# Kernel tuning notes

Measured on AMD Instinct MI355X. Metric: run time of the kernel, lower is better.

The kernel has to match this reference:

```python
import jax, jax.numpy as jnp
import numpy as np

B, L, D, H, DFF, C = 16, 1024, 256, 4, 2048, 3
NS, NC = 4, 4
DH = D // H


def _ln(x, g, b):
    m = x.mean(-1, keepdims=True)
    v = ((x - m) ** 2).mean(-1, keepdims=True)
    return (x - m) / jnp.sqrt(v + 1e-5) * g + b


def setup_inputs() -> dict:
    key = jax.random.key(0)
    ks = jax.random.split(key, 24)
    n = lambda k, s: jax.random.normal(k, s, jnp.float32) * 0.02
    return {
        'shape_idxs': jax.random.randint(ks[0], (B, L), 0, NS, jnp.int32),
        'color_idxs': jax.random.randint(ks[1], (B, L), 0, NC, jnp.int32),
        'shape_emb': n(ks[2], (NS, D)),
        'color_emb': n(ks[3], (NC, D)),
        'Wq': n(ks[4], (D, D)), 'bq': jnp.zeros((D,)),
        'Wk': n(ks[5], (D, D)), 'bk': jnp.zeros((D,)),
        'Wv': n(ks[6], (D, D)), 'bv': jnp.zeros((D,)),
        'Wo': n(ks[7], (D, D)), 'bo': jnp.zeros((D,)),
        'g1': jnp.ones((D,)), 'be1': jnp.zeros((D,)),
        'W1': n(ks[8], (D, DFF)), 'bf1': jnp.zeros((DFF,)),
        'W2': n(ks[9], (DFF, D)), 'bf2': jnp.zeros((D,)),
        'g2': jnp.ones((D,)), 'be2': jnp.zeros((D,)),
        'Wl': n(ks[10], (D, C)), 'bl': jnp.zeros((C,)),
        'Wp1': n(ks[11], (D, D)), 'bp1': jnp.zeros((D,)),
        'Wp2': n(ks[12], (D, 1)), 'bp2': jnp.zeros((1,)),
        'wc': n(ks[13], (1, 1)), 'bc': jnp.zeros((1,)),
    }


def reference(shape_idxs, color_idxs, shape_emb, color_emb, Wq, bq, Wk, bk, Wv, bv,
              Wo, bo, g1, be1, W1, bf1, W2, bf2, g2, be2, Wl, bl,
              Wp1, bp1, Wp2, bp2, wc, bc):
    # embed (dropout is identity in eval)
    x = shape_emb[shape_idxs] + color_emb[color_idxs]  # [B,L,D]
    # post-norm transformer encoder layer (PyTorch default)
    heads = lambda t: t.reshape(B, L, H, DH)
    q, k, v = heads(x @ Wq + bq), heads(x @ Wk + bk), heads(x @ Wv + bv)
    scores = jnp.einsum('blhd,bmhd->bhlm', q, k) / jnp.sqrt(jnp.float32(DH))
    attn = jax.nn.softmax(scores, axis=-1)
    ctx = jnp.einsum('bhlm,bmhd->blhd', attn, v).reshape(B, L, D)
    y = _ln(x + ctx @ Wo + bo, g1, be1)
    ff = jax.nn.relu(y @ W1 + bf1) @ W2 + bf2
    y = _ln(y + ff, g2, be2)  # trans_out [B,L,D]
    # latent logits / KL(prior || probs) with batchmean reduction
    logits = y @ Wl + bl
    logp = jax.nn.log_softmax(logits, axis=-1)
    prior = 1.0 / C
    kl_loss = jnp.sum(prior * (jnp.log(jnp.float32(prior)) - logp)) / B
    # data-dependent boundary segmentation (argmax of probs == argmax of logits)
    boundaries = (jnp.argmax(logits, axis=-1) == 0)
    boundaries = boundaries.at[:, 0].set(True)
    closed = boundaries & (jnp.arange(L) > 0)  # closure at l>0 ends segment at l
    seg_id = jnp.cumsum(closed.astype(jnp.int32), axis=1) - closed  # exclusive cumsum
    gid = (jnp.arange(B)[:, None] * L + seg_id).reshape(-1)  # global segment ids
    sums = jax.ops.segment_sum(y.reshape(B * L, D), gid, num_segments=B * L)
    counts = jax.ops.segment_sum(jnp.ones((B * L,), jnp.float32), gid, num_segments=B * L)
    means = sums / jnp.maximum(counts, 1.0)[:, None]  # per-segment mean [B*L,D]
    # predicate net + composition, mean over valid segments
    preds = jax.nn.sigmoid(jax.nn.relu(means @ Wp1 + bp1) @ Wp2 + bp2)  # [B*L,1]
    comp = (preds * wc[0, 0] + bc[0]).reshape(B, L)
    valid = (counts > 0).reshape(B, L).astype(jnp.float32)
    mean_comp = jnp.sum(comp * valid, axis=1) / jnp.sum(valid, axis=1)
    final_scores = jax.nn.sigmoid(mean_comp)
    return final_scores, kl_loss
```

## Files before the change

### kernel.cpp

```cpp
#include <hip/hip_runtime.h>


typedef unsigned short u16;
typedef u16    u16x4  __attribute__((ext_vector_type(4)));
typedef u16    u16x8  __attribute__((ext_vector_type(8)));
typedef __bf16 bf16x8 __attribute__((ext_vector_type(8)));
typedef float  f32x4  __attribute__((ext_vector_type(4)));

__device__ __forceinline__ float bf2f(u16 u) {
    union { unsigned int i; float f; } v; v.i = ((unsigned int)u) << 16; return v.f;
}
__device__ __forceinline__ u16 f2bf(float f) {
    union { float f; unsigned int i; } v; v.f = f;
    unsigned int r = (v.i + 0x7FFFu + ((v.i >> 16) & 1u)) >> 16;
    return (u16)r;
}
__device__ __forceinline__ u16 f2bf_fast(float f) {
    union { __bf16 h; u16 u; } v; v.h = (__bf16)f; return v.u;
}
__device__ __forceinline__ void gll16(const u16* g, u16* l) {
    __builtin_amdgcn_global_load_lds((__attribute__((address_space(1))) void*)(u16*)g,
                                     (__attribute__((address_space(3))) void*)l, 16, 0, 0);
}

__global__ void k_dzero(int* __restrict__ diag) {
    if (threadIdx.x < 16) diag[threadIdx.x] = 0;
}
__global__ __launch_bounds__(256) void k_detect(const u16* __restrict__ w1raw,
                                                int* __restrict__ diag) {
    int i = blockIdx.x * 256 + threadIdx.x;
    int bad = 0;
    for (int k = i; k < 65536; k += 64 * 256) {
        unsigned v = w1raw[k] & 0x7FFFu;
        if (v >= 0x7F80u) bad++;
    }
    for (int off = 32; off >= 1; off >>= 1) bad += __shfl_xor(bad, off);
    __shared__ int bs[4];
    if ((threadIdx.x & 63) == 0) bs[threadIdx.x >> 6] = bad;
    __syncthreads();
    if (threadIdx.x == 0) {
        int tot = bs[0] + bs[1] + bs[2] + bs[3];
        if (tot) atomicAdd(&diag[14], tot);
        __threadfence();
        int ticket = atomicAdd(&diag[13], 1);
        if (ticket == 63) {
            int cnt = atomicAdd(&diag[14], 0);
            diag[15] = (cnt > 16) ? 1 : 0;
        }
    }
}

struct IngestTab {
    const void* src[26];
    unsigned    dstoff[26];
    int         n[26];
    float       scale[26];
};
__global__ __launch_bounds__(256) void k_ingest(IngestTab tab, u16* __restrict__ ing,
                                                const int* __restrict__ diag) {
    int t = blockIdx.y;
    int n = tab.n[t];
    int m = diag[15];
    float sc = tab.scale[t];
    u16* dst = ing + tab.dstoff[t];
    for (int i = blockIdx.x * 256 + threadIdx.x; i < n; i += gridDim.x * 256) {
        float v = m ? ((const float*)tab.src[t])[i] : bf2f(((const u16*)tab.src[t])[i]);
        dst[i] = f2bf(v * sc);
    }
}
__global__ void k_sentinel_f32(float* __restrict__ out, int code) {
    int t = threadIdx.x;
    if (t < 17) out[t] = (float)code;
}

struct TransTab {
    const u16* src[7];
    u16*       dst[7];
    int        K[7], N[7];
    int        tstart[8];
};
__global__ __launch_bounds__(256) void k_trans_all(TransTab tt) {
    __shared__ u16 tile[32][33];
    int bx = blockIdx.x;
    int wgt = 0;
#pragma unroll
    for (int i = 1; i < 7; ++i) if (bx >= tt.tstart[i]) wgt = i;
    int local = bx - tt.tstart[wgt];
    int K = tt.K[wgt], N = tt.N[wgt];
    int ntx = N >> 5;
    int txt = local % ntx, tyt = local / ntx;
    const u16* W = tt.src[wgt];
    u16* Wt = tt.dst[wgt];
    int tx = threadIdx.x & 31, ty = threadIdx.x >> 5;
    int n = txt * 32 + tx;
    for (int i = ty; i < 32; i += 8) {
        int k = tyt * 32 + i;
        tile[i][tx] = W[(size_t)k * N + n];
    }
    __syncthreads();
    int k2 = tyt * 32 + tx;
    for (int i = ty; i < 32; i += 8) {
        int n2 = txt * 32 + i;
        Wt[(size_t)n2 * K + k2] = tile[tx][i];
    }
}

__global__ __launch_bounds__(256) void k_vt(const u16* __restrict__ QKV,
                                            u16* __restrict__ VT) {
    __shared__ u16 tile[32][33];
    int tx = threadIdx.x & 31, ty = threadIdx.x >> 5;
    int bh = blockIdx.y >> 1, dh = blockIdx.y & 1;
    int b = bh >> 2, h = bh & 3;
    int l0 = blockIdx.x * 32, d0 = dh * 32;
    const u16* src = QKV + (size_t)(b * 1024 + l0) * 768 + 512 + h * 64 + d0;
    for (int i = ty; i < 32; i += 8)
        tile[i][tx] = src[(size_t)i * 768 + tx];
    __syncthreads();
    u16* dst = VT + (size_t)(bh * 64 + d0) * 1024 + l0;
    for (int i = ty; i < 32; i += 8)
        dst[(size_t)i * 1024 + tx] = tile[tx][i];
}

__global__ __launch_bounds__(256) void k_embed(const int* __restrict__ si,
                                               const int* __restrict__ ci,
                                               const u16* __restrict__ se,
                                               const u16* __restrict__ ce,
                                               u16* __restrict__ X) {
    int t = blockIdx.x * 256 + threadIdx.x;
    int row = t >> 5, seg = (t & 31) * 8;
    int s = si[row], c = ci[row];
    u16x8 a = *(const u16x8*)&se[s * 256 + seg];
    u16x8 b = *(const u16x8*)&ce[c * 256 + seg];
    u16x8 o;
#pragma unroll
    for (int e = 0; e < 8; ++e) o[e] = f2bf(bf2f(a[e]) + bf2f(b[e]));
    *(u16x8*)&X[(size_t)row * 256 + seg] = o;
}

__global__ __launch_bounds__(256) void k_gemm_bt(const u16* __restrict__ A,
                                                 const u16* __restrict__ Bt,
                                                 const u16* __restrict__ bias,
                                                 u16* __restrict__ C,
                                                 int N, int K, int relu, int gx) {
    __shared__ u16 As[128][32];
    __shared__ u16 Bs[128][32];
    const int tid = threadIdx.x;
    const int xcd = blockIdx.x & 7, j = blockIdx.x >> 3;
    const int m0 = (xcd * 16 + j / gx) * 128, n0 = (j % gx) * 128;
    const int lane = tid & 63, wid = tid >> 6;
    const int wm = (wid & 1) * 64, wn = (wid >> 1) * 64;
    const int m16 = lane & 15, quad = lane >> 4;
    f32x4 acc[4][4] = {};
    const int arow = tid >> 2;
    const int ac8  = (tid & 3) * 8;
    const u16* Ap0 = A  + (size_t)(m0 + arow) * K + ac8;
    const u16* Ap1 = A  + (size_t)(m0 + 64 + arow) * K + ac8;
    const u16* Bp0 = Bt + (size_t)(n0 + arow) * K + ac8;
    const u16* Bp1 = Bt + (size_t)(n0 + 64 + arow) * K + ac8;
    u16* lA0 = &As[arow][ac8];
    u16* lA1 = &As[64 + arow][ac8];
    u16* lB0 = &Bs[arow][ac8];
    u16* lB1 = &Bs[64 + arow][ac8];

    for (int k0 = 0; k0 < K; k0 += 32) {
        __syncthreads();
        gll16(Ap0 + k0, lA0);
        gll16(Ap1 + k0, lA1);
        gll16(Bp0 + k0, lB0);
        gll16(Bp1 + k0, lB1);
        __syncthreads();
        bf16x8 af[4], bfv[4];
#pragma unroll
        for (int i = 0; i < 4; ++i)
            af[i] = *(const bf16x8*)&As[wm + i * 16 + m16][quad * 8];
#pragma unroll
        for (int j2 = 0; j2 < 4; ++j2)
            bfv[j2] = *(const bf16x8*)&Bs[wn + j2 * 16 + m16][quad * 8];
#pragma unroll
        for (int i = 0; i < 4; ++i)
#pragma unroll
            for (int j2 = 0; j2 < 4; ++j2)
                acc[i][j2] = __builtin_amdgcn_mfma_f32_16x16x32_bf16(
                    af[i], bfv[j2], acc[i][j2], 0, 0, 0);
    }

#pragma unroll
    for (int i = 0; i < 4; ++i) {
        int row = m0 + wm + i * 16 + quad * 4;
#pragma unroll
        for (int j2 = 0; j2 < 4; ++j2) {
            int col = n0 + wn + j2 * 16 + m16;
            float bv = bf2f(bias[col]);
#pragma unroll
            for (int r = 0; r < 4; ++r) {
                float v = acc[i][j2][r] + bv;
                if (relu) v = fmaxf(v, 0.f);
                C[(size_t)(row + r) * N + col] = f2bf_fast(v);
            }
        }
    }
}

__global__ __launch_bounds__(256) void k_gemm64(const u16* __restrict__ A,
                                                const u16* __restrict__ Bt,
                                                const u16* __restrict__ bias,
                                                u16* __restrict__ C,
                                                int N, int K, int relu,
                                                int gx, int mtpx,
                                                const float* __restrict__ gate) {
    __shared__ u16 As0[64][32], As1[64][32];
    __shared__ u16 Bs0[128][32], Bs1[128][32];
    const int tid = threadIdx.x;
    const int xcd = blockIdx.x & 7, j = blockIdx.x >> 3;
    const int m0 = (xcd * mtpx + j / gx) * 64, n0 = (j % gx) * 128;
    if (gate && gate[m0] == 0.f) return;
    const int lane = tid & 63, wid = tid >> 6;
    const int wm = (wid & 1) * 32, wn = (wid >> 1) * 64;
    const int m16 = lane & 15, quad = lane >> 4;
    f32x4 acc[2][4] = {};
    const int arow = tid >> 2;
    const int ac8  = (tid & 3) * 8;
    const u16* Ap  = A  + (size_t)(m0 + arow) * K + ac8;
    const u16* Bp0 = Bt + (size_t)(n0 + arow) * K + ac8;
    const u16* Bp1 = Bt + (size_t)(n0 + 64 + arow) * K + ac8;
    u16* lA0  = &As0[arow][ac8];
    u16* lA1  = &As1[arow][ac8];
    u16* lB00 = &Bs0[arow][ac8];
    u16* lB01 = &Bs0[64 + arow][ac8];
    u16* lB10 = &Bs1[arow][ac8];
    u16* lB11 = &Bs1[64 + arow][ac8];

    for (int k0 = 0; k0 < K; k0 += 64) {
        __syncthreads();
        gll16(Ap + k0,        lA0);
        gll16(Ap + k0 + 32,   lA1);
        gll16(Bp0 + k0,       lB00);
        gll16(Bp0 + k0 + 32,  lB10);
        gll16(Bp1 + k0,       lB01);
        gll16(Bp1 + k0 + 32,  lB11);
        __syncthreads();
#pragma unroll
        for (int ks = 0; ks < 2; ++ks) {
            bf16x8 af[2], bfv[4];
#pragma unroll
            for (int i = 0; i < 2; ++i)
                af[i] = ks == 0 ? *(const bf16x8*)&As0[wm + i * 16 + m16][quad * 8]
                                : *(const bf16x8*)&As1[wm + i * 16 + m16][quad * 8];
#pragma unroll
            for (int j2 = 0; j2 < 4; ++j2)
                bfv[j2] = ks == 0 ? *(const bf16x8*)&Bs0[wn + j2 * 16 + m16][quad * 8]
                                  : *(const bf16x8*)&Bs1[wn + j2 * 16 + m16][quad * 8];
#pragma unroll
            for (int i = 0; i < 2; ++i)
#pragma unroll
                for (int j2 = 0; j2 < 4; ++j2)
                    acc[i][j2] = __builtin_amdgcn_mfma_f32_16x16x32_bf16(
                        af[i], bfv[j2], acc[i][j2], 0, 0, 0);
        }
    }

#pragma unroll
    for (int i = 0; i < 2; ++i) {
        int row = m0 + wm + i * 16 + quad * 4;
#pragma unroll
        for (int j2 = 0; j2 < 4; ++j2) {
            int col = n0 + wn + j2 * 16 + m16;
            float bv = bf2f(bias[col]);
#pragma unroll
            for (int r = 0; r < 4; ++r) {
                float v = acc[i][j2][r] + bv;
                if (relu) v = fmaxf(v, 0.f);
                C[(size_t)(row + r) * N + col] = f2bf_fast(v);
            }
        }
    }
}

__global__ __launch_bounds__(256) void k_attn_mfma(const u16* __restrict__ QKV,
                                                   const u16* __restrict__ VT,
                                                   u16* __restrict__ CTX) {
    __shared__ u16 Ks[64][72];
    __shared__ u16 Vts[64][72];
    __shared__ u16 Ps[4][16][72];
    const int tid = threadIdx.x, lane = tid & 63, w = tid >> 6;
    const int quad = lane >> 4, c = lane & 15;
    const int blk = blockIdx.x;
    const int xcd = blk & 7, local = blk >> 3;
    const int bh = xcd * 8 + (local >> 4);
    const int qt = local & 15;
    const int b = bh >> 2, h = bh & 3;
    const int qrow0 = b * 1024 + qt * 64;

    const u16* qptr = QKV + (size_t)(qrow0 + w * 16 + c) * 768 + h * 64;
    bf16x8 aq0 = *(const bf16x8*)(qptr + quad * 8);
    bf16x8 aq1 = *(const bf16x8*)(qptr + 32 + quad * 8);

    f32x4 acc_o[4] = {};
    float l_part[4] = {0.f, 0.f, 0.f, 0.f};

    const u16* kbase  = QKV + (size_t)(b * 1024) * 768 + 256 + h * 64;
    const u16* vtbase = VT + (size_t)(bh * 64) * 1024;
    const int skk = tid >> 3, sc8 = (tid & 7) * 8;

    for (int t = 0; t < 16; ++t) {
        __syncthreads();
#pragma unroll
        for (int it = 0; it < 2; ++it) {
            int rr = skk + 32 * it;
            *(u16x8*)&Ks[rr][sc8]  = *(const u16x8*)(kbase + (size_t)(t * 64 + rr) * 768 + sc8);
            *(u16x8*)&Vts[rr][sc8] = *(const u16x8*)(vtbase + (size_t)rr * 1024 + t * 64 + sc8);
        }
        __syncthreads();

        f32x4 s[4];
#pragma unroll
        for (int nt = 0; nt < 4; ++nt) {
            f32x4 z = {};
            bf16x8 bk0 = *(const bf16x8*)&Ks[nt * 16 + c][quad * 8];
            bf16x8 bk1 = *(const bf16x8*)&Ks[nt * 16 + c][32 + quad * 8];
            z = __builtin_amdgcn_mfma_f32_16x16x32_bf16(aq0, bk0, z, 0, 0, 0);
            s[nt] = __builtin_amdgcn_mfma_f32_16x16x32_bf16(aq1, bk1, z, 0, 0, 0);
        }

#pragma unroll
        for (int nt = 0; nt < 4; ++nt)
#pragma unroll
            for (int r = 0; r < 4; ++r) {
                float pv = exp2f(fminf(s[nt][r], 80.f));
                l_part[r] += pv;
                Ps[w][quad * 4 + r][nt * 16 + c] = f2bf_fast(pv);
            }

#pragma unroll
        for (int ks = 0; ks < 2; ++ks) {
            bf16x8 ap = *(const bf16x8*)&Ps[w][c][ks * 32 + quad * 8];
#pragma unroll
            for (int nt = 0; nt < 4; ++nt) {
                bf16x8 bv = *(const bf16x8*)&Vts[nt * 16 + c][ks * 32 + quad * 8];
                acc_o[nt] = __builtin_amdgcn_mfma_f32_16x16x32_bf16(ap, bv, acc_o[nt], 0, 0, 0);
            }
        }
    }

#pragma unroll
    for (int r = 0; r < 4; ++r) {
#pragma unroll
        for (int off = 1; off <= 8; off <<= 1) l_part[r] += __shfl_xor(l_part[r], off);
    }
#pragma unroll
    for (int nt = 0; nt < 4; ++nt) {
        int col = h * 64 + nt * 16 + c;
#pragma unroll
        for (int r = 0; r < 4; ++r) {
            int row = qrow0 + w * 16 + quad * 4 + r;
            CTX[(size_t)row * 256 + col] = f2bf_fast(acc_o[nt][r] / l_part[r]);
        }
    }
}

__global__ __launch_bounds__(256) void k_ln(const u16* __restrict__ A,
                                            const u16* __restrict__ R,
                                            const u16* __restrict__ g,
                                            const u16* __restrict__ be,
                                            u16* __restrict__ out) {
    int w = threadIdx.x >> 6, lane = threadIdx.x & 63;
    int row = blockIdx.x * 4 + w;
    size_t base = (size_t)row * 256 + lane * 4;
    u16x4 a4 = *(const u16x4*)&A[base];
    u16x4 r4 = *(const u16x4*)&R[base];
    float v[4];
    float s = 0.f, sq = 0.f;
#pragma unroll
    for (int j = 0; j < 4; ++j) {
        v[j] = bf2f(a4[j]) + bf2f(r4[j]);
        s += v[j]; sq += v[j] * v[j];
    }
    for (int off = 32; off >= 1; off >>= 1) { s += __shfl_xor(s, off); sq += __shfl_xor(sq, off); }
    float mean = s * (1.f / 256.f);
    float var  = sq * (1.f / 256.f) - mean * mean;
    float rs   = rsqrtf(var + 1e-5f);
    u16x4 o;
#pragma unroll
    for (int j = 0; j < 4; ++j) {
        int d = lane * 4 + j;
        o[j] = f2bf((v[j] - mean) * rs * bf2f(g[d]) + bf2f(be[d]));
    }
    *(u16x4*)&out[base] = o;
}

__global__ void k_zeroall(f32x4* __restrict__ sums, float* __restrict__ cntacc) {
    int i = blockIdx.x * 256 + threadIdx.x;
    for (int j = i; j < 1048576; j += gridDim.x * 256) { f32x4 z = {}; sums[j] = z; }
    if (i < 16448) cntacc[i] = 0.f;
}

__global__ __launch_bounds__(256) void k_logits(const u16* __restrict__ FFO,
                                                const u16* __restrict__ Y1,
                                                const u16* __restrict__ g2,
                                                const u16* __restrict__ be2,
                                                const u16* __restrict__ Wl,
                                                const u16* __restrict__ bl,
                                                u16* __restrict__ Y2,
                                                float* __restrict__ kl_acc,
                                                int* __restrict__ flags) {
    const int tid = threadIdx.x, lane = tid & 63, w = tid >> 6;
    float wv[4][3], gv[4], bev[4];
#pragma unroll
    for (int j = 0; j < 4; ++j) {
        int d = lane * 4 + j;
        gv[j]  = bf2f(g2[d]);
        bev[j] = bf2f(be2[d]);
#pragma unroll
        for (int c = 0; c < 3; ++c) wv[j][c] = bf2f(Wl[d * 3 + c]);
    }
    const float b0 = bf2f(bl[0]), b1 = bf2f(bl[1]), b2 = bf2f(bl[2]);
    float klsum = 0.f;
    const int row0 = blockIdx.x * 64 + w * 16;
    for (int i = 0; i < 16; ++i) {
        int row = row0 + i;
        size_t base = (size_t)row * 256 + lane * 4;
        u16x4 f4 = *(const u16x4*)&FFO[base];
        u16x4 y4 = *(const u16x4*)&Y1[base];
        float v[4];
        float s = 0.f, sq = 0.f;
#pragma unroll
        for (int j = 0; j < 4; ++j) {
            v[j] = bf2f(f4[j]) + bf2f(y4[j]);
            s += v[j]; sq += v[j] * v[j];
        }
        for (int off = 32; off >= 1; off >>= 1) { s += __shfl_xor(s, off); sq += __shfl_xor(sq, off); }
        float mean = s * (1.f / 256.f);
        float var  = sq * (1.f / 256.f) - mean * mean;
        float rs   = rsqrtf(var + 1e-5f);
        u16x4 o;
        float a0 = 0.f, a1 = 0.f, a2 = 0.f;
#pragma unroll
        for (int j = 0; j < 4; ++j) {
            float yn = (v[j] - mean) * rs * gv[j] + bev[j];
            o[j] = f2bf(yn);
            float y = bf2f(o[j]);
            a0 += y * wv[j][0]; a1 += y * wv[j][1]; a2 += y * wv[j][2];
        }
        *(u16x4*)&Y2[base] = o;
        for (int off = 32; off >= 1; off >>= 1) {
            a0 += __shfl_xor(a0, off); a1 += __shfl_xor(a1, off); a2 += __shfl_xor(a2, off);
        }
        if (lane == 0) {
            float l0 = a0 + b0, l1 = a1 + b1, l2 = a2 + b2;
            float mx = fmaxf(l0, fmaxf(l1, l2));
            float lse = mx + __logf(__expf(l0 - mx) + __expf(l1 - mx) + __expf(l2 - mx));
            klsum += lse - (l0 + l1 + l2) * (1.f / 3.f) - 1.0986122886681098f;
            int am = 0; float bv = l0;
            if (l1 > bv) { bv = l1; am = 1; }
            if (l2 > bv) { am = 2; }
            int l = row & 1023;
            flags[row] = (am == 0 && l != 0) ? 1 : 0;
        }
    }
    __shared__ float kls[4];
    if (lane == 0) kls[w] = klsum;
    __syncthreads();
    if (tid == 0) atomicAdd(kl_acc, kls[0] + kls[1] + kls[2] + kls[3]);
}

__global__ void k_scan(const int* __restrict__ flags, int* __restrict__ seg) {
    __shared__ int wsum[16];
    int b = blockIdx.x, t = threadIdx.x;
    int lane = t & 63, w = t >> 6;
    int f = flags[b * 1024 + t];
    int x = f;
#pragma unroll
    for (int off = 1; off < 64; off <<= 1) {
        int v = __shfl_up(x, off);
        if (lane >= off) x += v;
    }
    if (lane == 63) wsum[w] = x;
    __syncthreads();
    if (w == 0) {
        int s = (lane < 16) ? wsum[lane] : 0;
#pragma unroll
        for (int off = 1; off < 16; off <<= 1) {
            int v = __shfl_up(s, off);
            if (lane >= off) s += v;
        }
        if (lane < 16) wsum[lane] = s;
    }
    __syncthreads();
    int prefix = (w > 0) ? wsum[w - 1] : 0;
    seg[b * 1024 + t] = prefix + x - f;
}

__global__ __launch_bounds__(256) void k_scatter(const u16* __restrict__ Y,
                                                 const int* __restrict__ seg,
                                                 float* __restrict__ sums,
                                                 float* __restrict__ cnt) {
    const int chunk = blockIdx.x;
    const int d = threadIdx.x;
    const int row0 = chunk * 16;
    const int b = row0 >> 10;
    float acc = 0.f;
    int runLen = 0;
    int s = seg[row0];
    for (int i = 0; i < 16; ++i) {
        int row = row0 + i;
        acc += bf2f(Y[(size_t)row * 256 + d]);
        runLen++;
        int end;
        if (i == 15) end = 1;
        else { int s2 = seg[row + 1]; end = (s2 != s); }
        if (end) {
            atomicAdd(&sums[(size_t)(b * 1024 + s) * 256 + d], acc);
            if (d == 0) atomicAdd(&cnt[b * 1024 + s], (float)runLen);
            acc = 0.f; runLen = 0;
            if (i < 15) s = seg[row + 1];
        }
    }
}

__global__ __launch_bounds__(64) void k_means(const float* __restrict__ sums,
                                              const float* __restrict__ cnt,
                                              u16* __restrict__ means) {
    int g = blockIdx.x, lane = threadIdx.x;
    float c = cnt[g];
    if (c == 0.f) return;
    float inv = 1.f / c;
    f32x4 v = *(const f32x4*)&sums[(size_t)g * 256 + lane * 4];
    u16x4 o;
#pragma unroll
    for (int j = 0; j < 4; ++j) o[j] = f2bf(v[j] * inv);
    *(u16x4*)&means[(size_t)g * 256 + lane * 4] = o;
}

__global__ __launch_bounds__(256) void k_preds(const u16* __restrict__ T,
                                               const u16* __restrict__ Wp2,
                                               const u16* __restrict__ bp2,
                                               const u16* __restrict__ wc,
                                               const u16* __restrict__ bc,
                                               const float* __restrict__ cnt,
                                               float* __restrict__ num,
                                               float* __restrict__ den) {
    const int tid = threadIdx.x, lane = tid & 63, w = tid >> 6;
    float lwp[4];
#pragma unroll
    for (int j = 0; j < 4; ++j) lwp[j] = bf2f(Wp2[lane * 4 + j]);
    const float fb = bf2f(bp2[0]), fw = bf2f(wc[0]), fc = bf2f(bc[0]);
    float csum = 0.f, vsum = 0.f;
    const int g0 = blockIdx.x * 16 + w * 4;
    if (cnt[g0] != 0.f) {
        for (int i = 0; i < 4; ++i) {
            int g = g0 + i;
            u16x4 t4 = *(const u16x4*)&T[(size_t)g * 256 + lane * 4];
            float a = 0.f;
#pragma unroll
            for (int j = 0; j < 4; ++j) a += bf2f(t4[j]) * lwp[j];
            for (int off = 32; off >= 1; off >>= 1) a += __shfl_xor(a, off);
            if (lane == 0 && cnt[g] > 0.f) {
                float pred = 1.f / (1.f + __expf(-(a + fb)));
                csum += pred * fw + fc;
                vsum += 1.f;
            }
        }
    }
    __shared__ float cs[4], vs[4];
    if (lane == 0) { cs[w] = csum; vs[w] = vsum; }
    __syncthreads();
    if (tid == 0) {
        float c = cs[0] + cs[1] + cs[2] + cs[3];
        float v = vs[0] + vs[1] + vs[2] + vs[3];
        if (v > 0.f) {
            int b = (blockIdx.x * 16) >> 10;
            atomicAdd(&num[b], c);
            atomicAdd(&den[b], v);
        }
    }
}

__global__ void k_final(const float* __restrict__ num, const float* __restrict__ den,
                        const float* __restrict__ kl, const int* __restrict__ diag,
                        void* __restrict__ outv) {
    int t = threadIdx.x;
    if (t > 16) return;
    int mode = diag[15];
    float val;
    if (t < 16) {
        float d = den[t], nm = num[t];
        if (!(d > 0.f)) d = 1.f;
        if (isnan(nm) || isinf(nm)) nm = 0.f;
        val = 1.f / (1.f + __expf(-nm / d));
    } else {
        val = kl[0] * (1.f / 16.f);
        if (isnan(val) || isinf(val)) val = 0.f;
    }
    if (mode) ((float*)outv)[t] = val;
    else      ((u16*)outv)[t]   = f2bf(val);
}

extern "C" void kernel_launch(void* const* d_in, const int* in_sizes, int n_in,
                              void* d_out, int out_size, void* d_ws, size_t ws_size,
                              hipStream_t stream) {
    const int* shape_idxs = (const int*)d_in[0];
    const int* color_idxs = (const int*)d_in[1];
    char* ws = (char*)d_ws;
    const size_t MB = 1024 * 1024;

    if (ws_size < 90 * MB) {
        int wsMB = (int)(ws_size >> 20); if (wsMB > 250) wsMB = 250;
        k_sentinel_f32<<<1, 32, 0, stream>>>((float*)d_out, 200 + wsMB);
        return;
    }

    u16*   X     = (u16*)(ws);
    u16*   QKVb  = (u16*)(ws + 8 * MB);
    u16*   VT    = (u16*)(ws + 32 * MB);
    u16*   CTX   = (u16*)(ws + 40 * MB);
    u16*   CTXP  = (u16*)(ws + 48 * MB);
    u16*   Y1    = (u16*)(ws + 64 * MB);
    u16*   Hb    = (u16*)(ws);
    u16*   FFO   = (u16*)(ws + 72 * MB);
    u16*   Y2    = (u16*)(ws);
    float* SUMS  = (float*)(ws + 8 * MB);
    u16*   MEANS = (u16*)(ws + 24 * MB);
    u16*   TB    = (u16*)(ws + 32 * MB);
    int*   FLAGS = (int*)(ws + 80 * MB);
    int*   SEG   = (int*)(ws + 80 * MB + 65536);
    float* CNT   = (float*)(ws + 80 * MB + 131072);
    float* ACC   = (float*)(ws + 80 * MB + 196608);
    u16*   W3T   = (u16*)(ws + 81 * MB);
    u16*   WoT   = (u16*)(ws + 81 * MB + 786432);
    u16*   Wp1T  = (u16*)(ws + 81 * MB + 917504);
    u16*   W1T   = (u16*)(ws + 82 * MB);
    u16*   W2T   = (u16*)(ws + 83 * MB);
    int*   DIAG  = (int*)(ws + 84 * MB);
    u16*   ING   = (u16*)(ws + 85 * MB);

    static const int NS_[26] = {1024,1024,65536,256,65536,256,65536,256,65536,256,
                                256,256,524288,2048,524288,256,256,256,768,3,
                                65536,256,256,1,1,1};
    const float QSCALE = 0.125f * 1.44269504f;
    IngestTab tab;
    unsigned off = 0;
    for (int i = 0; i < 26; ++i) {
        tab.src[i] = d_in[2 + i];
        tab.n[i] = NS_[i];
        tab.scale[i] = 1.0f;
        if (i == 3) { tab.dstoff[3] = off; tab.dstoff[5] = off + 256; tab.dstoff[7] = off + 512; off += 768; }
        else if (i == 5 || i == 7) continue;
        else { tab.dstoff[i] = off; off += (unsigned)((NS_[i] + 8) & ~7); }
    }
    tab.scale[2] = QSCALE;
    tab.scale[3] = QSCALE;
    const u16* iSE  = ING + tab.dstoff[0];  const u16* iCE  = ING + tab.dstoff[1];
    const u16* iWq  = ING + tab.dstoff[2];  const u16* ib3  = ING + tab.dstoff[3];
    const u16* iWk  = ING + tab.dstoff[4];
    const u16* iWv  = ING + tab.dstoff[6];
    const u16* iWo  = ING + tab.dstoff[8];  const u16* ibo  = ING + tab.dstoff[9];
    const u16* ig1  = ING + tab.dstoff[10]; const u16* ibe1 = ING + tab.dstoff[11];
    const u16* iW1  = ING + tab.dstoff[12]; const u16* ibf1 = ING + tab.dstoff[13];
    const u16* iW2  = ING + tab.dstoff[14]; const u16* ibf2 = ING + tab.dstoff[15];
    const u16* ig2  = ING + tab.dstoff[16]; const u16* ibe2 = ING + tab.dstoff[17];
    const u16* iWl  = ING + tab.dstoff[18]; const u16* ibl  = ING + tab.dstoff[19];
    const u16* iWp1 = ING + tab.dstoff[20]; const u16* ibp1 = ING + tab.dstoff[21];
    const u16* iWp2 = ING + tab.dstoff[22]; const u16* ibp2 = ING + tab.dstoff[23];
    const u16* iwc  = ING + tab.dstoff[24]; const u16* ibc  = ING + tab.dstoff[25];

    k_dzero<<<1, 16, 0, stream>>>(DIAG);
    k_detect<<<64, 256, 0, stream>>>((const u16*)d_in[14], DIAG);
    k_ingest<<<dim3(256, 26), 256, 0, stream>>>(tab, ING, DIAG);

    TransTab tt;
    const u16* tsrc[7] = {iWq, iWk, iWv, iWo, iWp1, iW1, iW2};
    u16* tdst[7] = {W3T, W3T + 256 * 256, W3T + 512 * 256, WoT, Wp1T, W1T, W2T};
    int tK[7] = {256, 256, 256, 256, 256, 256, 2048};
    int tN[7] = {256, 256, 256, 256, 256, 2048, 256};
    int ts = 0;
    for (int i = 0; i < 7; ++i) {
        tt.src[i] = tsrc[i]; tt.dst[i] = tdst[i]; tt.K[i] = tK[i]; tt.N[i] = tN[i];
        tt.tstart[i] = ts;
        ts += (tK[i] >> 5) * (tN[i] >> 5);
    }
    tt.tstart[7] = ts;
    k_trans_all<<<ts, 256, 0, stream>>>(tt);

    k_embed<<<2048, 256, 0, stream>>>(shape_idxs, color_idxs, iSE, iCE, X);
    k_gemm64<<<1536, 256, 0, stream>>>(X, W3T, ib3, QKVb, 768, 256, 0, 6, 32, nullptr);
    k_vt<<<dim3(32, 128), 256, 0, stream>>>(QKVb, VT);
    k_attn_mfma<<<1024, 256, 0, stream>>>(QKVb, VT, CTX);
    k_gemm64<<<512, 256, 0, stream>>>(CTX, WoT, ibo, CTXP, 256, 256, 0, 2, 32, nullptr);
    k_ln<<<4096, 256, 0, stream>>>(CTXP, X, ig1, ibe1, Y1);
    k_gemm_bt<<<16 * 128, 256, 0, stream>>>(Y1, W1T, ibf1, Hb, 2048, 256, 1, 16);
    k_gemm64<<<512, 256, 0, stream>>>(Hb, W2T, ibf2, FFO, 256, 2048, 0, 2, 32, nullptr);
    k_zeroall<<<1024, 256, 0, stream>>>((f32x4*)SUMS, CNT);
    k_logits<<<256, 256, 0, stream>>>(FFO, Y1, ig2, ibe2, iWl, ibl, Y2, ACC, FLAGS);
    k_scan<<<16, 1024, 0, stream>>>(FLAGS, SEG);
    k_scatter<<<1024, 256, 0, stream>>>(Y2, SEG, SUMS, CNT);
    k_means<<<16384, 64, 0, stream>>>(SUMS, CNT, MEANS);
    k_gemm64<<<512, 256, 0, stream>>>(MEANS, Wp1T, ibp1, TB, 256, 256, 1, 2, 32, CNT);
    k_preds<<<1024, 256, 0, stream>>>(TB, iWp2, ibp2, iwc, ibc, CNT, ACC + 1, ACC + 17);
    k_final<<<1, 32, 0, stream>>>(ACC + 1, ACC + 17, ACC, DIAG, d_out);
}
```

Before: 340.8 us.

## Fuse V-transpose into QKV GEMM and replace segment scatter with binary-search means

Writes the V portion of the QKV GEMM output directly in transposed layout, which removes the separate k_vt transpose kernel. Replaces the zero-fill, atomic scatter and means kernels with a single k_segmean kernel that finds each segment's row range by binary search over the segment ids and sums the rows directly. The KL partial sums move from one atomic to a per-block array that k_final reduces, and k_logits runs with more, smaller blocks. Together these remove a 16 MB zero-fill, the float atomics and several launches, at the cost of 4-element strided VT writes and serial per-segment row loops.

```diff
diff --git a/kernel.cpp b/kernel.cpp
--- a/kernel.cpp
+++ b/kernel.cpp
@@ -23,8 +23,10 @@
                                      (__attribute__((address_space(3))) void*)l, 16, 0, 0);
 }
 
-__global__ void k_dzero(int* __restrict__ diag) {
-    if (threadIdx.x < 16) diag[threadIdx.x] = 0;
+__global__ void k_dzero(int* __restrict__ diag, float* __restrict__ acc) {
+    int t = threadIdx.x;
+    if (t < 16) diag[t] = 0;
+    if (t < 33) acc[t] = 0.f;
 }
 __global__ __launch_bounds__(256) void k_detect(const u16* __restrict__ w1raw,
                                                 int* __restrict__ diag) {
@@ -103,22 +105,6 @@
         int n2 = txt * 32 + i;
         Wt[(size_t)n2 * K + k2] = tile[tx][i];
     }
-}
-
-__global__ __launch_bounds__(256) void k_vt(const u16* __restrict__ QKV,
-                                            u16* __restrict__ VT) {
-    __shared__ u16 tile[32][33];
-    int tx = threadIdx.x & 31, ty = threadIdx.x >> 5;
-    int bh = blockIdx.y >> 1, dh = blockIdx.y & 1;
-    int b = bh >> 2, h = bh & 3;
-    int l0 = blockIdx.x * 32, d0 = dh * 32;
-    const u16* src = QKV + (size_t)(b * 1024 + l0) * 768 + 512 + h * 64 + d0;
-    for (int i = ty; i < 32; i += 8)
-        tile[i][tx] = src[(size_t)i * 768 + tx];
-    __syncthreads();
-    u16* dst = VT + (size_t)(bh * 64 + d0) * 1024 + l0;
-    for (int i = ty; i < 32; i += 8)
-        dst[(size_t)i * 1024 + tx] = tile[tx][i];
 }
 
 __global__ __launch_bounds__(256) void k_embed(const int* __restrict__ si,
@@ -207,13 +193,15 @@
                                                 u16* __restrict__ C,
                                                 int N, int K, int relu,
                                                 int gx, int mtpx,
-                                                const float* __restrict__ gate) {
+                                                const float* __restrict__ gate,
+                                                u16* __restrict__ vt) {
     __shared__ u16 As0[64][32], As1[64][32];
     __shared__ u16 Bs0[128][32], Bs1[128][32];
     const int tid = threadIdx.x;
     const int xcd = blockIdx.x & 7, j = blockIdx.x >> 3;
     const int m0 = (xcd * mtpx + j / gx) * 64, n0 = (j % gx) * 128;
     if (gate && gate[m0] == 0.f) return;
+    const int vmode = (vt != nullptr) && (n0 >= 512);
     const int lane = tid & 63, wid = tid >> 6;
     const int wm = (wid & 1) * 32, wn = (wid >> 1) * 64;
     const int m16 = lane & 15, quad = lane >> 4;
@@ -266,11 +254,21 @@
         for (int j2 = 0; j2 < 4; ++j2) {
             int col = n0 + wn + j2 * 16 + m16;
             float bv = bf2f(bias[col]);
-#pragma unroll
-            for (int r = 0; r < 4; ++r) {
-                float v = acc[i][j2][r] + bv;
-                if (relu) v = fmaxf(v, 0.f);
-                C[(size_t)(row + r) * N + col] = f2bf_fast(v);
+            if (vmode) {
+                int ch = col - 512;
+                u16x4 o;
+#pragma unroll
+                for (int r = 0; r < 4; ++r) o[r] = f2bf_fast(acc[i][j2][r] + bv);
+                size_t vb = ((size_t)((row >> 10) * 4 + (ch >> 6)) * 64 + (ch & 63)) * 1024
+                          + (row & 1023);
+                *(u16x4*)&vt[vb] = o;
+            } else {
+#pragma unroll
+                for (int r = 0; r < 4; ++r) {
+                    float v = acc[i][j2][r] + bv;
+                    if (relu) v = fmaxf(v, 0.f);
+                    C[(size_t)(row + r) * N + col] = f2bf_fast(v);
+                }
             }
         }
     }
@@ -388,12 +386,6 @@
     *(u16x4*)&out[base] = o;
 }
 
-__global__ void k_zeroall(f32x4* __restrict__ sums, float* __restrict__ cntacc) {
-    int i = blockIdx.x * 256 + threadIdx.x;
-    for (int j = i; j < 1048576; j += gridDim.x * 256) { f32x4 z = {}; sums[j] = z; }
-    if (i < 16448) cntacc[i] = 0.f;
-}
-
 __global__ __launch_bounds__(256) void k_logits(const u16* __restrict__ FFO,
                                                 const u16* __restrict__ Y1,
                                                 const u16* __restrict__ g2,
@@ -401,7 +393,7 @@
                                                 const u16* __restrict__ Wl,
                                                 const u16* __restrict__ bl,
                                                 u16* __restrict__ Y2,
-                                                float* __restrict__ kl_acc,
+                                                float* __restrict__ klpart,
                                                 int* __restrict__ flags) {
     const int tid = threadIdx.x, lane = tid & 63, w = tid >> 6;
     float wv[4][3], gv[4], bev[4];
@@ -415,8 +407,8 @@
     }
     const float b0 = bf2f(bl[0]), b1 = bf2f(bl[1]), b2 = bf2f(bl[2]);
     float klsum = 0.f;
-    const int row0 = blockIdx.x * 64 + w * 16;
-    for (int i = 0; i < 16; ++i) {
+    const int row0 = blockIdx.x * 16 + w * 4;
+    for (int i = 0; i < 4; ++i) {
         int row = row0 + i;
         size_t base = (size_t)row * 256 + lane * 4;
         u16x4 f4 = *(const u16x4*)&FFO[base];
@@ -460,7 +452,7 @@
     __shared__ float kls[4];
     if (lane == 0) kls[w] = klsum;
     __syncthreads();
-    if (tid == 0) atomicAdd(kl_acc, kls[0] + kls[1] + kls[2] + kls[3]);
+    if (tid == 0) klpart[blockIdx.x] = kls[0] + kls[1] + kls[2] + kls[3];
 }
 
 __global__ void k_scan(const int* __restrict__ flags, int* __restrict__ seg) {
@@ -490,44 +482,34 @@
     seg[b * 1024 + t] = prefix + x - f;
 }
 
-__global__ __launch_bounds__(256) void k_scatter(const u16* __restrict__ Y,
-                                                 const int* __restrict__ seg,
-                                                 float* __restrict__ sums,
-                                                 float* __restrict__ cnt) {
-    const int chunk = blockIdx.x;
-    const int d = threadIdx.x;
-    const int row0 = chunk * 16;
-    const int b = row0 >> 10;
-    float acc = 0.f;
-    int runLen = 0;
-    int s = seg[row0];
-    for (int i = 0; i < 16; ++i) {
-        int row = row0 + i;
-        acc += bf2f(Y[(size_t)row * 256 + d]);
-        runLen++;
-        int end;
-        if (i == 15) end = 1;
-        else { int s2 = seg[row + 1]; end = (s2 != s); }
-        if (end) {
-            atomicAdd(&sums[(size_t)(b * 1024 + s) * 256 + d], acc);
-            if (d == 0) atomicAdd(&cnt[b * 1024 + s], (float)runLen);
-            acc = 0.f; runLen = 0;
-            if (i < 15) s = seg[row + 1];
-        }
-    }
-}
-
-__global__ __launch_bounds__(64) void k_means(const float* __restrict__ sums,
-                                              const float* __restrict__ cnt,
-                                              u16* __restrict__ means) {
+__global__ __launch_bounds__(64) void k_segmean(const u16* __restrict__ Y,
+                                                const int* __restrict__ seg,
+                                                u16* __restrict__ means,
+                                                float* __restrict__ cnt) {
     int g = blockIdx.x, lane = threadIdx.x;
-    float c = cnt[g];
-    if (c == 0.f) return;
-    float inv = 1.f / c;
-    f32x4 v = *(const f32x4*)&sums[(size_t)g * 256 + lane * 4];
+    int b = g >> 10, s = g & 1023;
+    const int* sb = seg + b * 1024;
+    int target = s + (lane & 1);
+    int lo = 0, hi = 1024;
+    while (lo < hi) {
+        int mid = (lo + hi) >> 1;
+        if (sb[mid] < target) lo = mid + 1; else hi = mid;
+    }
+    int start = __shfl(lo, 0);
+    int end   = __shfl(lo, 1);
+    int n = end - start;
+    if (lane == 0) cnt[g] = (float)n;
+    if (n <= 0) return;
+    f32x4 acc = {};
+    for (int row = start; row < end; ++row) {
+        u16x4 y4 = *(const u16x4*)&Y[(size_t)(b * 1024 + row) * 256 + lane * 4];
+        acc[0] += bf2f(y4[0]); acc[1] += bf2f(y4[1]);
+        acc[2] += bf2f(y4[2]); acc[3] += bf2f(y4[3]);
+    }
+    float inv = 1.f / (float)n;
     u16x4 o;
 #pragma unroll
-    for (int j = 0; j < 4; ++j) o[j] = f2bf(v[j] * inv);
+    for (int j = 0; j < 4; ++j) o[j] = f2bf(acc[j] * inv);
     *(u16x4*)&means[(size_t)g * 256 + lane * 4] = o;
 }
 
@@ -576,9 +558,13 @@
 }
 
 __global__ void k_final(const float* __restrict__ num, const float* __restrict__ den,
-                        const float* __restrict__ kl, const int* __restrict__ diag,
+                        const float* __restrict__ klp, const int* __restrict__ diag,
                         void* __restrict__ outv) {
     int t = threadIdx.x;
+    float k = 0.f;
+    for (int i = t; i < 1024; i += 64) k += klp[i];
+    for (int off = 32; off >= 1; off >>= 1) k += __shfl_xor(k, off);
+    float ktot = __shfl(k, 0);
     if (t > 16) return;
     int mode = diag[15];
     float val;
@@ -588,7 +574,7 @@
         if (isnan(nm) || isinf(nm)) nm = 0.f;
         val = 1.f / (1.f + __expf(-nm / d));
     } else {
-        val = kl[0] * (1.f / 16.f);
+        val = ktot * (1.f / 16.f);
         if (isnan(val) || isinf(val)) val = 0.f;
     }
     if (mode) ((float*)outv)[t] = val;
@@ -618,13 +604,13 @@
     u16*   Hb    = (u16*)(ws);
     u16*   FFO   = (u16*)(ws + 72 * MB);
     u16*   Y2    = (u16*)(ws);
-    float* SUMS  = (float*)(ws + 8 * MB);
     u16*   MEANS = (u16*)(ws + 24 * MB);
     u16*   TB    = (u16*)(ws + 32 * MB);
     int*   FLAGS = (int*)(ws + 80 * MB);
     int*   SEG   = (int*)(ws + 80 * MB + 65536);
     float* CNT   = (float*)(ws + 80 * MB + 131072);
     float* ACC   = (float*)(ws + 80 * MB + 196608);
+    float* KLP   = (float*)(ws + 80 * MB + 262144);
     u16*   W3T   = (u16*)(ws + 81 * MB);
     u16*   WoT   = (u16*)(ws + 81 * MB + 786432);
     u16*   Wp1T  = (u16*)(ws + 81 * MB + 917504);
@@ -663,7 +649,7 @@
     const u16* iWp2 = ING + tab.dstoff[22]; const u16* ibp2 = ING + tab.dstoff[23];
     const u16* iwc  = ING + tab.dstoff[24]; const u16* ibc  = ING + tab.dstoff[25];
 
-    k_dzero<<<1, 16, 0, stream>>>(DIAG);
+    k_dzero<<<1, 64, 0, stream>>>(DIAG, ACC);
     k_detect<<<64, 256, 0, stream>>>((const u16*)d_in[14], DIAG);
     k_ingest<<<dim3(256, 26), 256, 0, stream>>>(tab, ING, DIAG);
 
@@ -682,19 +668,16 @@
     k_trans_all<<<ts, 256, 0, stream>>>(tt);
 
     k_embed<<<2048, 256, 0, stream>>>(shape_idxs, color_idxs, iSE, iCE, X);
-    k_gemm64<<<1536, 256, 0, stream>>>(X, W3T, ib3, QKVb, 768, 256, 0, 6, 32, nullptr);
-    k_vt<<<dim3(32, 128), 256, 0, stream>>>(QKVb, VT);
+    k_gemm64<<<1536, 256, 0, stream>>>(X, W3T, ib3, QKVb, 768, 256, 0, 6, 32, nullptr, VT);
     k_attn_mfma<<<1024, 256, 0, stream>>>(QKVb, VT, CTX);
-    k_gemm64<<<512, 256, 0, stream>>>(CTX, WoT, ibo, CTXP, 256, 256, 0, 2, 32, nullptr);
+    k_gemm64<<<512, 256, 0, stream>>>(CTX, WoT, ibo, CTXP, 256, 256, 0, 2, 32, nullptr, nullptr);
     k_ln<<<4096, 256, 0, stream>>>(CTXP, X, ig1, ibe1, Y1);
     k_gemm_bt<<<16 * 128, 256, 0, stream>>>(Y1, W1T, ibf1, Hb, 2048, 256, 1, 16);
-    k_gemm64<<<512, 256, 0, stream>>>(Hb, W2T, ibf2, FFO, 256, 2048, 0, 2, 32, nullptr);
-    k_zeroall<<<1024, 256, 0, stream>>>((f32x4*)SUMS, CNT);
-    k_logits<<<256, 256, 0, stream>>>(FFO, Y1, ig2, ibe2, iWl, ibl, Y2, ACC, FLAGS);
+    k_gemm64<<<512, 256, 0, stream>>>(Hb, W2T, ibf2, FFO, 256, 2048, 0, 2, 32, nullptr, nullptr);
+    k_logits<<<1024, 256, 0, stream>>>(FFO, Y1, ig2, ibe2, iWl, ibl, Y2, KLP, FLAGS);
     k_scan<<<16, 1024, 0, stream>>>(FLAGS, SEG);
-    k_scatter<<<1024, 256, 0, stream>>>(Y2, SEG, SUMS, CNT);
-    k_means<<<16384, 64, 0, stream>>>(SUMS, CNT, MEANS);
-    k_gemm64<<<512, 256, 0, stream>>>(MEANS, Wp1T, ibp1, TB, 256, 256, 1, 2, 32, CNT);
+    k_segmean<<<16384, 64, 0, stream>>>(Y2, SEG, MEANS, CNT);
+    k_gemm64<<<512, 256, 0, stream>>>(MEANS, Wp1T, ibp1, TB, 256, 256, 1, 2, 32, CNT, nullptr);
     k_preds<<<1024, 256, 0, stream>>>(TB, iWp2, ibp2, iwc, ibc, CNT, ACC + 1, ACC + 17);
-    k_final<<<1, 32, 0, stream>>>(ACC + 1, ACC + 17, ACC, DIAG, d_out);
-}
+    k_final<<<1, 64, 0, stream>>>(ACC + 1, ACC + 17, KLP, DIAG, d_out);
+}
```

Measured after the change: 321.4 us. 5.7% less time.
